# Performance work log

Hardware: AMD Instinct MI355X
Metric: run time of the kernel (lower is better)

The kernel has to match this reference:

```python
import jax, jax.numpy as jnp
import numpy as np

D_MODEL = 1024
N_HEADS = 16
D_HEAD = D_MODEL // N_HEADS
SCALE = 1.0 / np.sqrt(D_HEAD)  # mup=False -> 1/sqrt(d_head)


def setup_inputs() -> dict:
    key = jax.random.key(0)
    ks = jax.random.split(key, 5)
    B, T, C = 4, 2048, D_MODEL
    s = 0.02
    return {
        "x": jax.random.normal(ks[0], (B, T, C), dtype=jnp.float32),
        "W_qkv": jax.random.normal(ks[1], (C, 3 * C), dtype=jnp.float32) * s,
        "b_qkv": jnp.zeros((3 * C,), dtype=jnp.float32),
        "W_proj": jax.random.normal(ks[2], (C, C), dtype=jnp.float32) * s,
        "b_proj": jnp.zeros((C,), dtype=jnp.float32),
    }


def reference(x, W_qkv, b_qkv, W_proj, b_proj):
    B, T, C = x.shape
    qkv = x @ W_qkv + b_qkv                      # [B,T,3C]
    q, k, v = jnp.split(qkv, 3, axis=-1)
    # [B,T,H,Dh] -> [B,H,T,Dh]
    q = q.reshape(B, T, N_HEADS, D_HEAD).transpose(0, 2, 1, 3)
    k = k.reshape(B, T, N_HEADS, D_HEAD).transpose(0, 2, 1, 3)
    v = v.reshape(B, T, N_HEADS, D_HEAD).transpose(0, 2, 1, 3)
    att = jnp.einsum("bhqd,bhkd->bhqk", q, k) * SCALE  # [B,H,T,T]
    causal = jnp.tril(jnp.ones((T, T), dtype=bool))
    att = jnp.where(causal, att, -jnp.inf)
    att = jax.nn.softmax(att, axis=-1)
    y = jnp.einsum("bhqk,bhkd->bhqd", att, v)    # [B,H,T,Dh]
    y = y.transpose(0, 2, 1, 3).reshape(B, T, C)
    return y @ W_proj + b_proj
```

## Files before the change

### kernel.cpp

```cpp
#include <hip/hip_runtime.h>

typedef unsigned short us;
typedef short bf16x8 __attribute__((ext_vector_type(8)));
typedef float f32x4 __attribute__((ext_vector_type(4)));
typedef float f32x16 __attribute__((ext_vector_type(16)));
typedef int i32x4 __attribute__((ext_vector_type(4)));

#define MFMA16(a, b, c) __builtin_amdgcn_mfma_f32_16x16x32_bf16(a, b, c, 0, 0, 0)
#define MFMA32(a, b, c) __builtin_amdgcn_mfma_f32_32x32x16_bf16(a, b, c, 0, 0, 0)

typedef const unsigned int __attribute__((address_space(1)))* gp_t;
typedef unsigned int __attribute__((address_space(3)))* lp_t;

__device__ __forceinline__ void gload16(const void* g, void* l) {
  __builtin_amdgcn_global_load_lds((gp_t)g, (lp_t)l, 16, 0, 0);
}

__device__ __forceinline__ us f2bf(float f) {
  unsigned u = __float_as_uint(f);
  u += 0x7fffu + ((u >> 16) & 1u);
  return (us)(u >> 16);
}

__device__ __forceinline__ unsigned cvtpk(float lo, float hi) {
  unsigned r;
  asm("v_cvt_pk_bf16_f32 %0, %1, %2" : "=v"(r) : "v"(lo), "v"(hi));
  return r;
}

__device__ __forceinline__ void plswap(unsigned& a, unsigned& b) {
  auto r = __builtin_amdgcn_permlane32_swap(a, b, false, false);
  a = r[0];
  b = r[1];
}

__device__ __forceinline__ float xsum32(float x) {
  unsigned u = __float_as_uint(x);
  auto r = __builtin_amdgcn_permlane32_swap(u, u, false, false);
  return __uint_as_float(r[0]) + __uint_as_float(r[1]);
}

__global__ __launch_bounds__(256) void k_conv(const float* __restrict__ in,
                                              us* __restrict__ out, int n4) {
  int i = blockIdx.x * 256 + threadIdx.x;
  if (i >= n4) return;
  float4 f = reinterpret_cast<const float4*>(in)[i];
  ushort4 o;
  o.x = f2bf(f.x); o.y = f2bf(f.y); o.z = f2bf(f.z); o.w = f2bf(f.w);
  reinterpret_cast<ushort4*>(out)[i] = o;
}

__global__ __launch_bounds__(256) void k_transconv(const float* __restrict__ W,
                                                   us* __restrict__ Wt, int K, int N) {
  __shared__ float tile[32][33];
  int nbn = N >> 5;
  int kt = blockIdx.x / nbn, nt = blockIdx.x - kt * nbn;
  int tx = threadIdx.x & 31, ty = threadIdx.x >> 5;
#pragma unroll
  for (int j = 0; j < 4; ++j)
    tile[ty + 8 * j][tx] = W[(size_t)(kt * 32 + ty + 8 * j) * N + nt * 32 + tx];
  __syncthreads();
#pragma unroll
  for (int j = 0; j < 4; ++j)
    Wt[(size_t)(nt * 32 + ty + 8 * j) * K + kt * 32 + tx] = f2bf(tile[tx][ty + 8 * j]);
}

template <int N, int EPI, int MINW>
__global__ __launch_bounds__(256, MINW) void k_gemm2(
    const us* __restrict__ A, const us* __restrict__ Bt,
    const float* __restrict__ bias, float* __restrict__ outf, us* __restrict__ qo,
    us* __restrict__ ko, us* __restrict__ vo) {
  constexpr int NBN = N / 128;
  constexpr int NWG = 64 * NBN;
  constexpr float QSC = 0.125f * 1.44269504088896f;
  int id = (blockIdx.x & 7) * (NWG / 8) + (blockIdx.x >> 3);
  int bm = id / NBN, bn = id % NBN;
  int lane = threadIdx.x & 63, wv = threadIdx.x >> 6;
  int wm = wv >> 1, wn = wv & 1;
  int c = lane & 31, h = lane >> 5;

  __shared__ __attribute__((aligned(16))) us As[128 * 64];
  __shared__ __attribute__((aligned(16))) us Bs[128 * 64];

  const us* Ag = A + (size_t)(bm * 128) * 1024;
  const us* Bg = Bt + (size_t)(bn * 128) * 1024;

  int sl = lane >> 3, scol = 8 * ((lane & 7) ^ sl);
  int swz = (c & 7) << 4;
  int rA0 = wm * 64 + c, rB0 = wn * 64 + c;
  int wv4 = wv * 4;

  f32x16 acc[2][2] = {};

  for (int k0 = 0; k0 < 1024; k0 += 64) {
#pragma unroll
    for (int t = 0; t < 4; ++t) {
      int i = wv4 + t;
      gload16(Ag + (size_t)(i * 8 + sl) * 1024 + k0 + scol, As + i * 512);
    }
#pragma unroll
    for (int t = 0; t < 4; ++t) {
      int i = wv4 + t;
      gload16(Bg + (size_t)(i * 8 + sl) * 1024 + k0 + scol, Bs + i * 512);
    }
    __syncthreads();
    const char* Ac = (const char*)As;
    const char* Bc = (const char*)Bs;
#pragma unroll
    for (int ks = 0; ks < 4; ++ks) {
      int cb = (ks * 32 + h * 16) ^ swz;
      bf16x8 a0 = *(const bf16x8*)(Ac + rA0 * 128 + cb);
      bf16x8 a1 = *(const bf16x8*)(Ac + (rA0 + 32) * 128 + cb);
      bf16x8 b0 = *(const bf16x8*)(Bc + rB0 * 128 + cb);
      bf16x8 b1 = *(const bf16x8*)(Bc + (rB0 + 32) * 128 + cb);
      acc[0][0] = MFMA32(a0, b0, acc[0][0]);
      acc[0][1] = MFMA32(a0, b1, acc[0][1]);
      acc[1][0] = MFMA32(a1, b0, acc[1][0]);
      acc[1][1] = MFMA32(a1, b1, acc[1][1]);
    }
    __syncthreads();
  }

#pragma unroll
  for (int mf = 0; mf < 2; ++mf) {
#pragma unroll
    for (int nf = 0; nf < 2; ++nf) {
      int gm0 = bm * 128 + wm * 64 + mf * 32 + 4 * h;
      int gn = bn * 128 + wn * 64 + nf * 32 + c;
      float bv = bias[gn];
      if (EPI == 0) {
        int which = gn >> 10, cc2 = gn & 1023;
        int hh = cc2 >> 6, dd = cc2 & 63;
        int b_ = gm0 >> 11, t0 = gm0 & 2047;
        if (which == 2) {
#pragma unroll
          for (int rr = 0; rr < 4; ++rr) {
            ushort4 o;
            o.x = f2bf(acc[mf][nf][4 * rr + 0] + bv);
            o.y = f2bf(acc[mf][nf][4 * rr + 1] + bv);
            o.z = f2bf(acc[mf][nf][4 * rr + 2] + bv);
            o.w = f2bf(acc[mf][nf][4 * rr + 3] + bv);
            *reinterpret_cast<ushort4*>(
                &vo[(((size_t)b_ * 16 + hh) * 64 + dd) * 2048 + t0 + 8 * rr]) = o;
          }
        } else {
          us* dst = which ? ko : qo;
          float sc2 = which ? 1.0f : QSC;
#pragma unroll
          for (int r = 0; r < 16; ++r) {
            int t_ = t0 + 8 * (r >> 2) + (r & 3);
            dst[(((size_t)b_ * 16 + hh) * 2048 + t_) * 64 + dd] =
                f2bf((acc[mf][nf][r] + bv) * sc2);
          }
        }
      } else {
#pragma unroll
        for (int r = 0; r < 16; ++r) {
          int gm = gm0 + 8 * (r >> 2) + (r & 3);
          outf[(size_t)gm * N + gn] = acc[mf][nf][r] + bv;
        }
      }
    }
  }
}

__global__ __launch_bounds__(256, 4) void k_attn3(const us* __restrict__ qg,
                                                  const us* __restrict__ kg,
                                                  const us* __restrict__ vT,
                                                  us* __restrict__ yb) {
  constexpr int T = 2048;
  __shared__ __attribute__((aligned(16))) us Ks[2][4096];
  __shared__ __attribute__((aligned(16))) us Vs[2][4096];
  int lane = threadIdx.x & 63;
  int wv = threadIdx.x >> 6;
  int b = blockIdx.x;
  int x = b & 7, y = b >> 3;
  int bh = x * 8 + (y & 7);
  int kk = y >> 3;
  int j2 = kk & 3, g2 = kk >> 2;
  int qt = (g2 == 0) ? (15 - 2 * j2)
         : (g2 == 1) ? (2 * j2)
         : (g2 == 2) ? (14 - 2 * j2)
                     : (2 * j2 + 1);
  int b_ = bh >> 4, hh = bh & 15;
  int c = lane & 31, h = lane >> 5;

  const us* Qb = qg + (size_t)bh * T * 64;
  const us* Kb = kg + (size_t)bh * T * 64;
  const us* Vb = vT + (size_t)bh * 64 * T;

  int nt = 2 * qt + 2;
  int tw = 2 * qt + (wv >> 1) + 1;
  int q0 = qt * 128 + wv * 32;
  int qrow = q0 + c;

  int sl = lane >> 3;
  int scol = 8 * ((lane & 7) ^ sl);
  int swl = (c & 7) << 4;

  bf16x8 qf[4];
#pragma unroll
  for (int ks = 0; ks < 4; ++ks)
    qf[ks] = *reinterpret_cast<const bf16x8*>(&Qb[(size_t)qrow * 64 + ks * 16 + h * 8]);

  f32x16 o0 = {}, o1 = {};
  float lsum = 0.f;

#pragma unroll
  for (int t = 0; t < 2; ++t) {
    int i = wv + 4 * t;
    gload16(Kb + (size_t)(i * 8 + sl) * 64 + scol, &Ks[0][i * 512]);
    gload16(Vb + (size_t)(i * 8 + sl) * T + scol, &Vs[0][i * 512]);
  }

  for (int j = 0; j < nt; ++j) {
    int buf = j & 1;
    __syncthreads();
    if (j + 1 < nt) {
      int j1 = (j + 1) * 64;
#pragma unroll
      for (int t = 0; t < 2; ++t) {
        int i = wv + 4 * t;
        gload16(Kb + (size_t)(j1 + i * 8 + sl) * 64 + scol, &Ks[buf ^ 1][i * 512]);
        gload16(Vb + (size_t)(i * 8 + sl) * T + j1 + scol, &Vs[buf ^ 1][i * 512]);
      }
    }
    if (j < tw) {
      int j0 = j * 64;
      const char* KsB = (const char*)Ks[buf];
      const char* VsB = (const char*)Vs[buf];
      f32x16 sA = {}, sB = {};
      __builtin_amdgcn_s_setprio(1);
#pragma unroll
      for (int ks = 0; ks < 4; ++ks) {
        int cb = (32 * ks + 16 * h) ^ swl;
        bf16x8 kfA = *reinterpret_cast<const bf16x8*>(KsB + c * 128 + cb);
        bf16x8 kfB = *reinterpret_cast<const bf16x8*>(KsB + (c + 32) * 128 + cb);
        sA = MFMA32(kfA, qf[ks], sA);
        sB = MFMA32(kfB, qf[ks], sB);
      }
      __builtin_amdgcn_s_setprio(0);
      if (j == tw - 1) {
#pragma unroll
        for (int r = 0; r < 16; ++r) {
          int kl = j0 + (r & 3) + 8 * (r >> 2) + 4 * h;
          if (kl > qrow) sA[r] = -1e30f;
          if (kl + 32 > qrow) sB[r] = -1e30f;
        }
      }
      float rs = 0.f;
#pragma unroll
      for (int r = 0; r < 16; ++r) {
        sA[r] = __builtin_amdgcn_exp2f(sA[r]);
        sB[r] = __builtin_amdgcn_exp2f(sB[r]);
        rs += sA[r] + sB[r];
      }
      lsum += rs;

#pragma unroll
      for (int hb = 0; hb < 4; ++hb) {
        int base = (hb & 1) * 8;
        unsigned w0, w1, w2, w3;
        if (hb < 2) {
          w0 = cvtpk(sA[base + 0], sA[base + 1]);
          w1 = cvtpk(sA[base + 2], sA[base + 3]);
          w2 = cvtpk(sA[base + 4], sA[base + 5]);
          w3 = cvtpk(sA[base + 6], sA[base + 7]);
        } else {
          w0 = cvtpk(sB[base + 0], sB[base + 1]);
          w1 = cvtpk(sB[base + 2], sB[base + 3]);
          w2 = cvtpk(sB[base + 4], sB[base + 5]);
          w3 = cvtpk(sB[base + 6], sB[base + 7]);
        }
        plswap(w0, w2);
        plswap(w1, w3);
        i32x4 pi;
        pi[0] = (int)w0; pi[1] = (int)w1; pi[2] = (int)w2; pi[3] = (int)w3;
        bf16x8 pa = __builtin_bit_cast(bf16x8, pi);
        int cb = (32 * hb + 16 * h) ^ swl;
        bf16x8 vf0 = *reinterpret_cast<const bf16x8*>(VsB + c * 128 + cb);
        bf16x8 vf1 = *reinterpret_cast<const bf16x8*>(VsB + (c + 32) * 128 + cb);
        __builtin_amdgcn_s_setprio(1);
        o0 = MFMA32(vf0, pa, o0);
        o1 = MFMA32(vf1, pa, o1);
        __builtin_amdgcn_s_setprio(0);
      }
    }
  }

  float inv = 1.0f / xsum32(lsum);
  size_t ob = ((size_t)b_ * T + qrow) * 1024 + (size_t)hh * 64;
#pragma unroll
  for (int r = 0; r < 16; r += 2) {
    int d = (r & 3) + 8 * (r >> 2) + 4 * h;
    *reinterpret_cast<unsigned*>(&yb[ob + d]) = cvtpk(o0[r] * inv, o0[r + 1] * inv);
    *reinterpret_cast<unsigned*>(&yb[ob + 32 + d]) = cvtpk(o1[r] * inv, o1[r + 1] * inv);
  }
}

extern "C" void kernel_launch(void* const* d_in, const int* in_sizes, int n_in,
                              void* d_out, int out_size, void* d_ws, size_t ws_size,
                              hipStream_t stream) {
  (void)in_sizes; (void)n_in; (void)out_size; (void)ws_size;
  const float* x = (const float*)d_in[0];
  const float* Wqkv = (const float*)d_in[1];
  const float* bqkv = (const float*)d_in[2];
  const float* Wproj = (const float*)d_in[3];
  const float* bproj = (const float*)d_in[4];
  float* out = (float*)d_out;

  char* ws = (char*)d_ws;
  us* xb = (us*)(ws);
  us* wqkvt = (us*)(ws + 16777216);
  us* wprojt = (us*)(ws + 23068672);
  us* qg = (us*)(ws + 25165824);
  us* kg = (us*)(ws + 41943040);
  us* vT = (us*)(ws + 58720256);
  us* yb = (us*)(ws + 75497472);

  k_conv<<<8192, 256, 0, stream>>>(x, xb, 2097152);
  k_transconv<<<3072, 256, 0, stream>>>(Wqkv, wqkvt, 1024, 3072);
  k_transconv<<<1024, 256, 0, stream>>>(Wproj, wprojt, 1024, 1024);
  k_gemm2<3072, 0, 3><<<1536, 256, 0, stream>>>(xb, wqkvt, bqkv, nullptr, qg, kg, vT);
  k_attn3<<<1024, 256, 0, stream>>>(qg, kg, vT, yb);
  k_gemm2<1024, 1, 2><<<512, 256, 0, stream>>>(yb, wprojt, bproj, out, nullptr, nullptr,
                                               nullptr);
}
```

Before: 160.6 us.

## Triple-buffer K/V tiles in attention with two-ahead prefetch and vmcnt waits

Converts the attention kernel's double-buffered K/V shared-memory staging into a three-slot ring that prefetches two tiles ahead. Each iteration waits only until the oldest outstanding loads have landed (vmcnt(4)) before the barrier, so more global-to-LDS traffic overlaps with the MFMA work. The cost is 50% more LDS per block (48KB), which may reduce occupancy at 4 blocks per CU. Past the last tile it issues dummy reloads of tile 0 into the free slot rather than branching around them.

```diff
diff --git a/kernel.cpp b/kernel.cpp
--- a/kernel.cpp
+++ b/kernel.cpp
@@ -169,8 +169,8 @@
                                                   const us* __restrict__ vT,
                                                   us* __restrict__ yb) {
   constexpr int T = 2048;
-  __shared__ __attribute__((aligned(16))) us Ks[2][4096];
-  __shared__ __attribute__((aligned(16))) us Vs[2][4096];
+  __shared__ __attribute__((aligned(16))) us Ks[3][4096];
+  __shared__ __attribute__((aligned(16))) us Vs[3][4096];
   int lane = threadIdx.x & 63;
   int wv = threadIdx.x >> 6;
   int b = blockIdx.x;
@@ -206,29 +206,32 @@
   f32x16 o0 = {}, o1 = {};
   float lsum = 0.f;
 
-#pragma unroll
-  for (int t = 0; t < 2; ++t) {
-    int i = wv + 4 * t;
-    gload16(Kb + (size_t)(i * 8 + sl) * 64 + scol, &Ks[0][i * 512]);
-    gload16(Vb + (size_t)(i * 8 + sl) * T + scol, &Vs[0][i * 512]);
-  }
-
+  auto STAGEJ = [&](int jt, int bsel) {
+    int j64 = jt * 64;
+#pragma unroll
+    for (int t = 0; t < 2; ++t) {
+      int i = wv + 4 * t;
+      gload16(Kb + (size_t)(j64 + i * 8 + sl) * 64 + scol, &Ks[bsel][i * 512]);
+      gload16(Vb + (size_t)(i * 8 + sl) * T + j64 + scol, &Vs[bsel][i * 512]);
+    }
+  };
+
+  STAGEJ(0, 0);
+  STAGEJ(1, 1);
+
+  int cur = 0, nx2 = 2;
   for (int j = 0; j < nt; ++j) {
-    int buf = j & 1;
-    __syncthreads();
-    if (j + 1 < nt) {
-      int j1 = (j + 1) * 64;
-#pragma unroll
-      for (int t = 0; t < 2; ++t) {
-        int i = wv + 4 * t;
-        gload16(Kb + (size_t)(j1 + i * 8 + sl) * 64 + scol, &Ks[buf ^ 1][i * 512]);
-        gload16(Vb + (size_t)(i * 8 + sl) * T + j1 + scol, &Vs[buf ^ 1][i * 512]);
-      }
+    asm volatile("s_waitcnt vmcnt(4)" ::: "memory");
+    __builtin_amdgcn_s_barrier();
+    __builtin_amdgcn_sched_barrier(0);
+    {
+      int jn = j + 2;
+      STAGEJ(jn < nt ? jn : 0, nx2);
     }
     if (j < tw) {
       int j0 = j * 64;
-      const char* KsB = (const char*)Ks[buf];
-      const char* VsB = (const char*)Vs[buf];
+      const char* KsB = (const char*)Ks[cur];
+      const char* VsB = (const char*)Vs[cur];
       f32x16 sA = {}, sB = {};
       __builtin_amdgcn_s_setprio(1);
 #pragma unroll
@@ -286,7 +289,10 @@
         __builtin_amdgcn_s_setprio(0);
       }
     }
+    cur = (cur + 1 < 3) ? cur + 1 : 0;
+    nx2 = (nx2 + 1 < 3) ? nx2 + 1 : 0;
   }
+  asm volatile("s_waitcnt vmcnt(0)" ::: "memory");
 
   float inv = 1.0f / xsum32(lsum);
   size_t ob = ((size_t)b_ * T + qrow) * 1024 + (size_t)hh * 64;
```

After: 174.7 us. +8.8%, slower.
